# Kernel optimization log

Measured on AMD Instinct MI355X. Metric: run time of the kernel, lower is better.

## Reference

```python
import jax, jax.numpy as jnp
import numpy as np

WS = 5   # window_size
VN = 8   # view_num -> H = W = VN*WS = 40


def _layernorm(x, g, b, eps=1e-5):
    mu = x.mean(-1, keepdims=True)
    var = ((x - mu) ** 2).mean(-1, keepdims=True)
    return (x - mu) * jax.lax.rsqrt(var + eps) * g + b


def _rel_index():
    # standard Swin relative-position index for a WS x WS window
    coords = np.stack(np.meshgrid(np.arange(WS), np.arange(WS), indexing='ij')).reshape(2, -1)
    rel = (coords[:, :, None] - coords[:, None, :]).transpose(1, 2, 0)  # (T,T,2)
    rel = rel + (WS - 1)
    return rel[:, :, 0] * (2 * WS - 1) + rel[:, :, 1]  # (T,T) int


def _attn_mask(H, W):
    # checkerboard mask: outer product of flattened per-window checkerboard,
    # 0 where both positions are 'on', -100 elsewhere (matches masked_fill logic)
    ckbd = np.zeros((H, W), np.float32)
    ckbd[0::2, 1::2] = 1.0
    ckbd[1::2, 0::2] = 1.0
    win = ckbd.reshape(VN, WS, VN, WS).transpose(0, 2, 1, 3).reshape(VN * VN, WS * WS)
    m = win[:, :, None] * win[:, None, :]  # (N,T,T)
    return np.where(m == 0.0, -100.0, 0.0).astype(np.float32)


def setup_inputs() -> dict:
    key = jax.random.key(0)
    ks = jax.random.split(key, 8)
    B, C, H, W = 64, 256, 40, 40
    nh = 8
    dim2 = 2 * C
    hid = int(dim2 * 2.0)

    def n(k, shape, s=0.02):
        return jax.random.normal(k, shape, jnp.float32) * s

    return dict(
        x=jax.random.normal(ks[0], (B, C, H, W), jnp.float32),
        qkv_w=n(ks[1], (C, 3 * C)), qkv_b=jnp.zeros((3 * C,), jnp.float32),
        rel_table=n(ks[2], ((2 * WS - 1) ** 2, nh)),
        proj_w=n(ks[3], (C, dim2)), proj_b=jnp.zeros((dim2,), jnp.float32),
        mlp_w1=n(ks[4], (dim2, hid)), mlp_b1=jnp.zeros((hid,), jnp.float32),
        mlp_w2=n(ks[5], (hid, dim2)), mlp_b2=jnp.zeros((dim2,), jnp.float32),
        norm1_g=jnp.ones((C,), jnp.float32), norm1_b=jnp.zeros((C,), jnp.float32),
        norm2_g=jnp.ones((dim2,), jnp.float32), norm2_b=jnp.zeros((dim2,), jnp.float32),
    )


def reference(x, qkv_w, qkv_b, rel_table, proj_w, proj_b,
              mlp_w1, mlp_b1, mlp_w2, mlp_b2,
              norm1_g, norm1_b, norm2_g, norm2_b):
    B, C, H, W = x.shape
    nh = rel_table.shape[1]
    hd = C // nh
    N = VN * VN           # windows
    T = WS * WS           # tokens per window
    scale = hd ** -0.5

    xs = _layernorm(x.reshape(B, C, H * W).transpose(0, 2, 1), norm1_g, norm1_b)  # (B,L,C)
    qkv = xs @ qkv_w + qkv_b                                   # (B,L,3C)
    qkv = qkv.reshape(B, H, W, 3, C).transpose(3, 0, 4, 1, 2)  # (3,B,C,H,W)
    # windowize: (3,B,C,u,ws,v,ws) -> (3,B,N,C,T)
    qkv = qkv.reshape(3, B, C, VN, WS, VN, WS).transpose(0, 1, 3, 5, 2, 4, 6).reshape(3, B, N, C, T)
    # NOTE: original splits C as (head_dim, num_heads) -- head index is MINOR
    qkv = qkv.reshape(3, B, N, hd, nh, T).transpose(0, 1, 2, 4, 5, 3)  # (3,B,N,nh,T,hd)
    q, k, v = qkv[0] * scale, qkv[1], qkv[2]

    attn = jnp.einsum('bnhtd,bnhsd->bnhts', q, k)              # (B,N,nh,T,T)
    bias = rel_table[jnp.asarray(_rel_index())].transpose(2, 0, 1)  # (nh,T,T)
    mask = jnp.asarray(_attn_mask(H, W))                       # (N,T,T)
    attn = jax.nn.softmax(attn + bias[None, None] + mask[None, :, None], axis=-1)

    out = jnp.einsum('bnhts,bnhsd->bnhtd', attn, v)            # (B,N,nh,T,hd)
    out = out.reshape(B, N, nh, WS, WS, hd).transpose(0, 1, 3, 4, 2, 5)  # (B,N,ws,ws,nh,hd)
    # 'B (u v) h w nh c -> B (u h v w) (nh c)'
    out = out.reshape(B, VN, VN, WS, WS, C).transpose(0, 1, 3, 2, 4, 5).reshape(B, H * W, C)

    y = out @ proj_w + proj_b                                  # (B,L,2C)
    h = _layernorm(y, norm2_g, norm2_b)
    h = jax.nn.gelu(h @ mlp_w1 + mlp_b1, approximate=False) @ mlp_w2 + mlp_b2
    y = y + h
    return y.transpose(0, 2, 1).reshape(B, -1, H, W)           # (B,2C,H,W)
```

## Files before the change

kernel.cpp:

```cpp
#include <hip/hip_runtime.h>
#include <math.h>

#define B_   64
#define C_   256
#define L_   1600
#define T_   25
#define ROWS (B_*L_)
#define QSCALE 0.17677669529663687f

typedef _Float16 f16;
typedef f16 f16x8 __attribute__((ext_vector_type(8)));
typedef f16 f16x4 __attribute__((ext_vector_type(4)));
typedef f16 f16x2 __attribute__((ext_vector_type(2)));
typedef float f32x4 __attribute__((ext_vector_type(4)));

__device__ __forceinline__ void gload_lds16(const void* g, void* l) {
  __builtin_amdgcn_global_load_lds(
      (const __attribute__((address_space(1))) unsigned int*)g,
      (__attribute__((address_space(3))) unsigned int*)l, 16, 0, 0);
}

__device__ __forceinline__ float dot8(f16x8 a, f16x8 b, float acc) {
  union U { f16x8 v; f16x2 p[4]; };
  U ua; ua.v = a;
  U ub; ub.v = b;
#pragma unroll
  for (int i = 0; i < 4; ++i)
    acc = __builtin_amdgcn_fdot2(ua.p[i], ub.p[i], acc, false);
  return acc;
}

__global__ __launch_bounds__(256) void wtrans(const float* __restrict__ w,
                                              f16* __restrict__ o, int K, int N) {
  __shared__ f16 tile[64][72];
  int tid = threadIdx.x;
  int n0 = blockIdx.x * 64, k0 = blockIdx.y * 64;
  int nn = tid & 63, kq = tid >> 6;
#pragma unroll
  for (int i = 0; i < 16; ++i) {
    int k = kq * 16 + i;
    tile[nn][k] = (f16)w[(size_t)(k0 + k) * N + n0 + nn];
  }
  __syncthreads();
#pragma unroll
  for (int jj = 0; jj < 2; ++jj) {
    int e = jj * 256 + tid;
    int nr = e >> 3, kb = e & 7;
    *(f16x8*)&o[(size_t)(n0 + nr) * K + k0 + kb * 8] = *(const f16x8*)&tile[nr][kb * 8];
  }
}

__global__ __launch_bounds__(256) void ln1_fused(const float* __restrict__ x,
    const float* __restrict__ g, const float* __restrict__ be,
    f16* __restrict__ xs) {
  __shared__ float t32[256][65];
  __shared__ float gL[256], beL[256];
  int tid = threadIdx.x;
  gL[tid] = g[tid]; beL[tid] = be[tid];
  int r0 = blockIdx.x * 64;
  int w = tid >> 6, rl = tid & 63;
  int grow = r0 + rl;
  int b = grow / L_, l = grow - b * L_;
  const float* xb = x + (size_t)b * (C_ * L_) + l;
#pragma unroll
  for (int i = 0; i < 64; ++i) {
    int c = w + i * 4;
    t32[c][rl] = xb[(size_t)c * L_];
  }
  __syncthreads();
  int row = tid >> 2, q = tid & 3;
  float s = 0.f, s2 = 0.f;
#pragma unroll
  for (int i = 0; i < 64; ++i) {
    float vv = t32[q * 64 + i][row];
    s += vv; s2 += vv * vv;
  }
  s += __shfl_xor(s, 1); s2 += __shfl_xor(s2, 1);
  s += __shfl_xor(s, 2); s2 += __shfl_xor(s2, 2);
  float m = s * (1.0f / 256.0f);
  float rr = rsqrtf(s2 * (1.0f / 256.0f) - m * m + 1e-5f);
  f16* orow = &xs[(size_t)(r0 + row) * 256 + q * 64];
#pragma unroll
  for (int z8 = 0; z8 < 8; ++z8) {
    f16x8 ov;
#pragma unroll
    for (int z = 0; z < 8; ++z) {
      int c = q * 64 + z8 * 8 + z;
      ov[z] = (f16)((t32[c][row] - m) * rr * gL[c] + beL[c]);
    }
    *(f16x8*)(orow + z8 * 8) = ov;
  }
}

template<int K, int N, int EPI>
__global__ __launch_bounds__(256) void gemm16(
    const f16* __restrict__ A, const f16* __restrict__ BT,
    const float* __restrict__ bias,
    float* __restrict__ outF, f16* __restrict__ outH,
    const f16* __restrict__ resid, int row_off) {
  __shared__ __align__(16) char smem[(EPI == 3) ? 64 * 129 * 4 : 16384];
  f16* As = (f16*)smem;
  f16* Bs = (f16*)(smem + 8192);
  float* tT = (float*)smem;
  int tid = threadIdx.x;
  int w = tid >> 6, lane = tid & 63;
  int wr = w >> 1, wc = w & 1;
  int r0 = blockIdx.y * 128;
  int n0 = blockIdx.x * 128;

  f32x4 acc[4][4] = {};

  for (int k0 = 0; k0 < K; k0 += 32) {
#pragma unroll
    for (int i = 0; i < 2; ++i) {
      int e = i * 256 + tid;
      int row = e >> 2, t = e & 3;
      int cb = t ^ ((row >> 1) & 3);
      gload_lds16(A + (size_t)(r0 + row) * K + k0 + cb * 8,
                  &As[(i * 4 + w) * 512]);
    }
#pragma unroll
    for (int i = 0; i < 2; ++i) {
      int e = i * 256 + tid;
      int row = e >> 2, t = e & 3;
      int cb = t ^ ((row >> 1) & 3);
      gload_lds16(BT + (size_t)(n0 + row) * K + k0 + cb * 8,
                  &Bs[(i * 4 + w) * 512]);
    }
    __syncthreads();

    f16x8 af[4], bf[4];
#pragma unroll
    for (int m = 0; m < 4; ++m) {
      int ar = wr * 64 + m * 16 + (lane & 15);
      int sl = (lane >> 4) ^ ((ar >> 1) & 3);
      af[m] = *(const f16x8*)&As[ar * 32 + sl * 8];
    }
#pragma unroll
    for (int n = 0; n < 4; ++n) {
      int br = wc * 64 + n * 16 + (lane & 15);
      int sl = (lane >> 4) ^ ((br >> 1) & 3);
      bf[n] = *(const f16x8*)&Bs[br * 32 + sl * 8];
    }
#pragma unroll
    for (int m = 0; m < 4; ++m)
#pragma unroll
      for (int n = 0; n < 4; ++n)
        acc[m][n] = __builtin_amdgcn_mfma_f32_16x16x32_f16(af[m], bf[n], acc[m][n], 0, 0, 0);
    __syncthreads();
  }

  if constexpr (EPI != 3) {
#pragma unroll
    for (int m = 0; m < 4; ++m) {
#pragma unroll
      for (int n = 0; n < 4; ++n) {
        int gcol = n0 + wc * 64 + n * 16 + (lane & 15);
        float bb = bias[gcol];
#pragma unroll
        for (int j = 0; j < 4; ++j) {
          int grow = r0 + wr * 64 + m * 16 + ((lane >> 4) << 2) + j;
          float v = acc[m][n][j] + bb;
          if constexpr (EPI == 0) {
            outH[(size_t)grow * N + gcol] = (f16)v;
          } else {
            float gl = 0.5f * v * (1.0f + erff(v * 0.70710678118654752f));
            outH[(size_t)grow * N + gcol] = (f16)gl;
          }
        }
      }
    }
  } else {
    for (int p = 0; p < 2; ++p) {
      if (wr == p) {
#pragma unroll
        for (int m = 0; m < 4; ++m) {
          int lr = m * 16 + ((lane >> 4) << 2);
#pragma unroll
          for (int n = 0; n < 4; ++n) {
            int lc = wc * 64 + n * 16 + (lane & 15);
            int gcol = n0 + lc;
            float bb = bias[gcol];
#pragma unroll
            for (int j = 0; j < 4; ++j) {
              int grow = row_off + r0 + p * 64 + lr + j;
              tT[(lr + j) * 129 + lc] =
                  acc[m][n][j] + bb + (float)resid[(size_t)grow * 512 + gcol];
            }
          }
        }
      }
      __syncthreads();
#pragma unroll
      for (int it = 0; it < 8; ++it) {
        int idx = it * 256 + tid;
        int col = idx >> 4;
        int r4 = idx & 15;
        int grow0 = row_off + r0 + p * 64 + r4 * 4;
        int b = grow0 / L_;
        int l = grow0 - b * L_;
        float4 o = make_float4(tT[(r4 * 4 + 0) * 129 + col],
                               tT[(r4 * 4 + 1) * 129 + col],
                               tT[(r4 * 4 + 2) * 129 + col],
                               tT[(r4 * 4 + 3) * 129 + col]);
        *(float4*)&outF[((size_t)b * 512 + n0 + col) * L_ + l] = o;
      }
      __syncthreads();
    }
  }
}

#define PST 776
__global__ __launch_bounds__(256) void attn_kernel(const f16* __restrict__ qkv,
                                                   const float* __restrict__ rel,
                                                   f16* __restrict__ outp) {
  __shared__ f16 qc[T_][PST];
  __shared__ f16 relL[81 * 8];
  int tid = threadIdx.x;
  int bn = blockIdx.x;
  int b = bn >> 6, n = bn & 63;
  int u = n >> 3, v = n & 7;

  for (int e = tid; e < 648; e += 256) relL[e] = (f16)rel[e];

  for (int e = tid; e < T_ * 96; e += 256) {
    int t = e / 96;
    int g = e - t * 96;
    int i = t / 5, j = t - i * 5;
    int l = (u * 5 + i) * 40 + v * 5 + j;
    f16x8 val = *(const f16x8*)&qkv[(size_t)(b * L_ + l) * 768 + g * 8];
    int which = g >> 5;
    int d = g & 31;
    int base = which * 256 + d;
#pragma unroll
    for (int h = 0; h < 8; ++h)
      qc[t][base + h * 32] = val[h];
  }
  __syncthreads();

  int h = tid >> 5, t = tid & 31;
  if (t < T_) {
    int i1 = t / 5, j1 = t - i1 * 5;
    int par1 = (u + v + i1 + j1) & 1;
    const f16* qp = &qc[t][h * 32];
    f16x8 q0 = *(const f16x8*)(qp + 0);
    f16x8 q1 = *(const f16x8*)(qp + 8);
    f16x8 q2 = *(const f16x8*)(qp + 16);
    f16x8 q3 = *(const f16x8*)(qp + 24);

    float p[T_];
    float mx = -1e30f;
#pragma unroll
    for (int s = 0; s < T_; ++s) {
      int i2 = s / 5, j2 = s - i2 * 5;
      const f16* kp = &qc[s][256 + h * 32];
      f16x8 k0 = *(const f16x8*)(kp + 0);
      f16x8 k1 = *(const f16x8*)(kp + 8);
      f16x8 k2 = *(const f16x8*)(kp + 16);
      f16x8 k3 = *(const f16x8*)(kp + 24);
      float d0 = 0.f, d1 = 0.f;
      d0 = dot8(q0, k0, d0);
      d1 = dot8(q1, k1, d1);
      d0 = dot8(q2, k2, d0);
      d1 = dot8(q3, k3, d1);
      float bias = (float)relL[((i1 - i2 + 4) * 9 + (j1 - j2 + 4)) * 8 + h];
      int par2 = (u + v + i2 + j2) & 1;
      float sc = (d0 + d1) * QSCALE + bias + ((par1 & par2) ? 0.0f : -100.0f);
      p[s] = sc;
      mx = fmaxf(mx, sc);
    }
    float sum = 0.f;
#pragma unroll
    for (int s = 0; s < T_; ++s) {
      float e = __expf(p[s] - mx);
      p[s] = e;
      sum += e;
    }
    float inv = 1.0f / sum;
#pragma unroll
    for (int s = 0; s < T_; ++s) p[s] *= inv;

    int l = (u * 5 + i1) * 40 + v * 5 + j1;
    f16* op = &outp[(size_t)(b * L_ + l) * 256 + h * 32];

#pragma unroll
    for (int half = 0; half < 2; ++half) {
      float acc[16] = {};
#pragma unroll
      for (int s = 0; s < T_; ++s) {
        const f16* vp = &qc[s][512 + h * 32 + half * 16];
        f16x8 v0 = *(const f16x8*)(vp + 0);
        f16x8 v1 = *(const f16x8*)(vp + 8);
        float ps = p[s];
#pragma unroll
        for (int z = 0; z < 8; ++z) {
          acc[z]     += ps * (float)v0[z];
          acc[8 + z] += ps * (float)v1[z];
        }
      }
#pragma unroll
      for (int z8 = 0; z8 < 2; ++z8) {
        f16x8 ov;
#pragma unroll
        for (int z = 0; z < 8; ++z) ov[z] = (f16)acc[z8 * 8 + z];
        *(f16x8*)(op + half * 16 + z8 * 8) = ov;
      }
    }
  }
}

__global__ __launch_bounds__(256) void ln2_fused(const f16* __restrict__ y,
    const float* __restrict__ g, const float* __restrict__ be,
    f16* __restrict__ yln) {
  int wv = threadIdx.x >> 6, lane = threadIdx.x & 63;
  int row = blockIdx.x * 4 + wv;
  const f16x8* yp = (const f16x8*)(y + (size_t)row * 512);
  f16x8 h0 = yp[lane];
  float v[8];
  float s = 0.f, s2 = 0.f;
#pragma unroll
  for (int z = 0; z < 8; ++z) {
    v[z] = (float)h0[z];
    s += v[z]; s2 += v[z] * v[z];
  }
#pragma unroll
  for (int o = 32; o; o >>= 1) { s += __shfl_xor(s, o); s2 += __shfl_xor(s2, o); }
  float m = s * (1.0f / 512.0f);
  float rr = rsqrtf(s2 * (1.0f / 512.0f) - m * m + 1e-5f);
  float4 g0 = ((const float4*)g)[lane * 2], g1 = ((const float4*)g)[lane * 2 + 1];
  float4 b0 = ((const float4*)be)[lane * 2], b1 = ((const float4*)be)[lane * 2 + 1];
  float gg[8] = {g0.x, g0.y, g0.z, g0.w, g1.x, g1.y, g1.z, g1.w};
  float bb[8] = {b0.x, b0.y, b0.z, b0.w, b1.x, b1.y, b1.z, b1.w};
  f16x8 o8;
#pragma unroll
  for (int z = 0; z < 8; ++z)
    o8[z] = (f16)((v[z] - m) * rr * gg[z] + bb[z]);
  *(f16x8*)&yln[(size_t)row * 512 + lane * 8] = o8;
}

extern "C" void kernel_launch(void* const* d_in, const int* in_sizes, int n_in,
                              void* d_out, int out_size, void* d_ws, size_t ws_size,
                              hipStream_t stream) {
  const float* x      = (const float*)d_in[0];
  const float* qkv_w  = (const float*)d_in[1];
  const float* qkv_b  = (const float*)d_in[2];
  const float* rel    = (const float*)d_in[3];
  const float* proj_w = (const float*)d_in[4];
  const float* proj_b = (const float*)d_in[5];
  const float* w1     = (const float*)d_in[6];
  const float* b1     = (const float*)d_in[7];
  const float* w2     = (const float*)d_in[8];
  const float* b2     = (const float*)d_in[9];
  const float* g1     = (const float*)d_in[10];
  const float* be1    = (const float*)d_in[11];
  const float* g2     = (const float*)d_in[12];
  const float* be2    = (const float*)d_in[13];
  float* out = (float*)d_out;

  char* w8 = (char*)d_ws;
  f16* qkv_wT  = (f16*)(w8 + 1638400);
  f16* proj_wT = qkv_wT + 768 * 256;
  f16* w1T     = proj_wT + 512 * 256;
  f16* w2T     = w1T + 1024 * 512;
  char* P0 = w8 + 4390912;
  f16* qkv_h = (f16*)P0;
  f16* y_h   = (f16*)P0;
  char* P1 = P0 + (size_t)ROWS * 768 * 2;
  f16* xs_h  = (f16*)P1;
  f16* att_h = (f16*)(P1 + (size_t)ROWS * 256 * 2);
  f16* yln   = (f16*)P1;
  char* P2 = P1 + (size_t)ROWS * 512 * 2;
  f16* hid = (f16*)P2;

  size_t need_full = 4390912 + (size_t)ROWS * 768 * 2 + (size_t)ROWS * 512 * 2
                   + (size_t)ROWS * 1024 * 2;
  bool full = ws_size >= need_full;

  wtrans<<<dim3(768 / 64, 256 / 64), 256, 0, stream>>>(qkv_w, qkv_wT, 256, 768);
  wtrans<<<dim3(512 / 64, 256 / 64), 256, 0, stream>>>(proj_w, proj_wT, 256, 512);
  wtrans<<<dim3(1024 / 64, 512 / 64), 256, 0, stream>>>(w1, w1T, 512, 1024);
  wtrans<<<dim3(512 / 64, 1024 / 64), 256, 0, stream>>>(w2, w2T, 1024, 512);

  ln1_fused<<<ROWS / 64, 256, 0, stream>>>(x, g1, be1, xs_h);

  gemm16<256, 768, 0><<<dim3(6, ROWS / 128), 256, 0, stream>>>(
      xs_h, qkv_wT, qkv_b, nullptr, qkv_h, nullptr, 0);

  attn_kernel<<<B_ * 64, 256, 0, stream>>>(qkv_h, rel, att_h);

  gemm16<256, 512, 0><<<dim3(4, ROWS / 128), 256, 0, stream>>>(
      att_h, proj_wT, proj_b, nullptr, y_h, nullptr, 0);

  ln2_fused<<<ROWS / 4, 256, 0, stream>>>(y_h, g2, be2, yln);

  if (full) {
    gemm16<512, 1024, 2><<<dim3(8, ROWS / 128), 256, 0, stream>>>(
        yln, w1T, b1, nullptr, hid, nullptr, 0);
    gemm16<1024, 512, 3><<<dim3(4, ROWS / 128), 256, 0, stream>>>(
        hid, w2T, b2, out, nullptr, y_h, 0);
  } else {
    const int CHUNK = ROWS / 4;
    for (int c = 0; c < 4; ++c) {
      int off = c * CHUNK;
      gemm16<512, 1024, 2><<<dim3(8, CHUNK / 128), 256, 0, stream>>>(
          yln + (size_t)off * 512, w1T, b1, nullptr, hid, nullptr, 0);
      gemm16<1024, 512, 3><<<dim3(4, CHUNK / 128), 256, 0, stream>>>(
          hid, w2T, b2, out, nullptr, y_h, off);
    }
  }
  (void)in_sizes; (void)n_in; (void)out_size;
}
```

Measured before the change: 783.1 us.

## Use 8-wave GEMM blocks with XCD-aware tile swizzle for L2 reuse

The fp16 MFMA GEMM now runs 512 threads per block. Each of the 8 waves computes a 64x32 sub-tile instead of 4 waves computing 64x64, so each thread issues a single LDS-direct load per operand per k-step. The 2D grid becomes a 1D grid that is remapped so consecutive blocks on the same XCD share a row tile. The goal is better reuse of the A operand in each XCD's L2 and more waves to hide latency. The trade-off is fewer MFMAs per fragment load per wave, which lowers register-level reuse.

```diff
diff --git a/kernel.cpp b/kernel.cpp
--- a/kernel.cpp
+++ b/kernel.cpp
@@ -92,44 +92,35 @@
   }
 }
 
-template<int K, int N, int EPI>
-__global__ __launch_bounds__(256) void gemm16(
+template<int K, int N, int EPI, int NCB>
+__global__ __launch_bounds__(512) void gemm16(
     const f16* __restrict__ A, const f16* __restrict__ BT,
     const float* __restrict__ bias,
     float* __restrict__ outF, f16* __restrict__ outH,
-    const f16* __restrict__ resid, int row_off) {
+    const f16* __restrict__ resid, int row_off, int nrp8) {
   __shared__ __align__(16) char smem[(EPI == 3) ? 64 * 129 * 4 : 16384];
   f16* As = (f16*)smem;
   f16* Bs = (f16*)(smem + 8192);
   float* tT = (float*)smem;
   int tid = threadIdx.x;
   int w = tid >> 6, lane = tid & 63;
-  int wr = w >> 1, wc = w & 1;
-  int r0 = blockIdx.y * 128;
-  int n0 = blockIdx.x * 128;
-
-  f32x4 acc[4][4] = {};
+  int wr = w >> 2, wc = w & 3;
+  int bid = blockIdx.x;
+  int xcd = bid & 7, j1d = bid >> 3;
+  int member = j1d % NCB, grp = j1d / NCB;
+  int r0 = (xcd * nrp8 + grp) * 128;
+  int n0 = member * 128;
+
+  f32x4 acc[4][2] = {};
+  int srow = tid >> 2, st = tid & 3;
+  int scb = st ^ ((srow >> 1) & 3);
 
   for (int k0 = 0; k0 < K; k0 += 32) {
-#pragma unroll
-    for (int i = 0; i < 2; ++i) {
-      int e = i * 256 + tid;
-      int row = e >> 2, t = e & 3;
-      int cb = t ^ ((row >> 1) & 3);
-      gload_lds16(A + (size_t)(r0 + row) * K + k0 + cb * 8,
-                  &As[(i * 4 + w) * 512]);
-    }
-#pragma unroll
-    for (int i = 0; i < 2; ++i) {
-      int e = i * 256 + tid;
-      int row = e >> 2, t = e & 3;
-      int cb = t ^ ((row >> 1) & 3);
-      gload_lds16(BT + (size_t)(n0 + row) * K + k0 + cb * 8,
-                  &Bs[(i * 4 + w) * 512]);
-    }
+    gload_lds16(A + (size_t)(r0 + srow) * K + k0 + scb * 8, &As[w * 512]);
+    gload_lds16(BT + (size_t)(n0 + srow) * K + k0 + scb * 8, &Bs[w * 512]);
     __syncthreads();
 
-    f16x8 af[4], bf[4];
+    f16x8 af[4], bf[2];
 #pragma unroll
     for (int m = 0; m < 4; ++m) {
       int ar = wr * 64 + m * 16 + (lane & 15);
@@ -137,15 +128,15 @@
       af[m] = *(const f16x8*)&As[ar * 32 + sl * 8];
     }
 #pragma unroll
-    for (int n = 0; n < 4; ++n) {
-      int br = wc * 64 + n * 16 + (lane & 15);
+    for (int n = 0; n < 2; ++n) {
+      int br = wc * 32 + n * 16 + (lane & 15);
       int sl = (lane >> 4) ^ ((br >> 1) & 3);
       bf[n] = *(const f16x8*)&Bs[br * 32 + sl * 8];
     }
 #pragma unroll
     for (int m = 0; m < 4; ++m)
 #pragma unroll
-      for (int n = 0; n < 4; ++n)
+      for (int n = 0; n < 2; ++n)
         acc[m][n] = __builtin_amdgcn_mfma_f32_16x16x32_f16(af[m], bf[n], acc[m][n], 0, 0, 0);
     __syncthreads();
   }
@@ -154,17 +145,17 @@
 #pragma unroll
     for (int m = 0; m < 4; ++m) {
 #pragma unroll
-      for (int n = 0; n < 4; ++n) {
-        int gcol = n0 + wc * 64 + n * 16 + (lane & 15);
+      for (int n = 0; n < 2; ++n) {
+        int gcol = n0 + wc * 32 + n * 16 + (lane & 15);
         float bb = bias[gcol];
 #pragma unroll
-        for (int j = 0; j < 4; ++j) {
-          int grow = r0 + wr * 64 + m * 16 + ((lane >> 4) << 2) + j;
-          float v = acc[m][n][j] + bb;
+        for (int j2 = 0; j2 < 4; ++j2) {
+          int grow = r0 + wr * 64 + m * 16 + ((lane >> 4) << 2) + j2;
+          float vv = acc[m][n][j2] + bb;
           if constexpr (EPI == 0) {
-            outH[(size_t)grow * N + gcol] = (f16)v;
+            outH[(size_t)grow * N + gcol] = (f16)vv;
           } else {
-            float gl = 0.5f * v * (1.0f + erff(v * 0.70710678118654752f));
+            float gl = 0.5f * vv * (1.0f + erff(vv * 0.70710678118654752f));
             outH[(size_t)grow * N + gcol] = (f16)gl;
           }
         }
@@ -177,23 +168,23 @@
         for (int m = 0; m < 4; ++m) {
           int lr = m * 16 + ((lane >> 4) << 2);
 #pragma unroll
-          for (int n = 0; n < 4; ++n) {
-            int lc = wc * 64 + n * 16 + (lane & 15);
+          for (int n = 0; n < 2; ++n) {
+            int lc = wc * 32 + n * 16 + (lane & 15);
             int gcol = n0 + lc;
             float bb = bias[gcol];
 #pragma unroll
-            for (int j = 0; j < 4; ++j) {
-              int grow = row_off + r0 + p * 64 + lr + j;
-              tT[(lr + j) * 129 + lc] =
-                  acc[m][n][j] + bb + (float)resid[(size_t)grow * 512 + gcol];
+            for (int j2 = 0; j2 < 4; ++j2) {
+              int grow = row_off + r0 + p * 64 + lr + j2;
+              tT[(lr + j2) * 129 + lc] =
+                  acc[m][n][j2] + bb + (float)resid[(size_t)grow * 512 + gcol];
             }
           }
         }
       }
       __syncthreads();
 #pragma unroll
-      for (int it = 0; it < 8; ++it) {
-        int idx = it * 256 + tid;
+      for (int it = 0; it < 4; ++it) {
+        int idx = it * 512 + tid;
         int col = idx >> 4;
         int r4 = idx & 15;
         int grow0 = row_off + r0 + p * 64 + r4 * 4;
@@ -383,29 +374,29 @@
 
   ln1_fused<<<ROWS / 64, 256, 0, stream>>>(x, g1, be1, xs_h);
 
-  gemm16<256, 768, 0><<<dim3(6, ROWS / 128), 256, 0, stream>>>(
-      xs_h, qkv_wT, qkv_b, nullptr, qkv_h, nullptr, 0);
+  gemm16<256, 768, 0, 6><<<6 * (ROWS / 128), 512, 0, stream>>>(
+      xs_h, qkv_wT, qkv_b, nullptr, qkv_h, nullptr, 0, (ROWS / 128) / 8);
 
   attn_kernel<<<B_ * 64, 256, 0, stream>>>(qkv_h, rel, att_h);
 
-  gemm16<256, 512, 0><<<dim3(4, ROWS / 128), 256, 0, stream>>>(
-      att_h, proj_wT, proj_b, nullptr, y_h, nullptr, 0);
+  gemm16<256, 512, 0, 4><<<4 * (ROWS / 128), 512, 0, stream>>>(
+      att_h, proj_wT, proj_b, nullptr, y_h, nullptr, 0, (ROWS / 128) / 8);
 
   ln2_fused<<<ROWS / 4, 256, 0, stream>>>(y_h, g2, be2, yln);
 
   if (full) {
-    gemm16<512, 1024, 2><<<dim3(8, ROWS / 128), 256, 0, stream>>>(
-        yln, w1T, b1, nullptr, hid, nullptr, 0);
-    gemm16<1024, 512, 3><<<dim3(4, ROWS / 128), 256, 0, stream>>>(
-        hid, w2T, b2, out, nullptr, y_h, 0);
+    gemm16<512, 1024, 2, 8><<<8 * (ROWS / 128), 512, 0, stream>>>(
+        yln, w1T, b1, nullptr, hid, nullptr, 0, (ROWS / 128) / 8);
+    gemm16<1024, 512, 3, 4><<<4 * (ROWS / 128), 512, 0, stream>>>(
+        hid, w2T, b2, out, nullptr, y_h, 0, (ROWS / 128) / 8);
   } else {
     const int CHUNK = ROWS / 4;
     for (int c = 0; c < 4; ++c) {
       int off = c * CHUNK;
-      gemm16<512, 1024, 2><<<dim3(8, CHUNK / 128), 256, 0, stream>>>(
-          yln + (size_t)off * 512, w1T, b1, nullptr, hid, nullptr, 0);
-      gemm16<1024, 512, 3><<<dim3(4, CHUNK / 128), 256, 0, stream>>>(
-          hid, w2T, b2, out, nullptr, y_h, off);
+      gemm16<512, 1024, 2, 8><<<8 * (CHUNK / 128), 512, 0, stream>>>(
+          yln + (size_t)off * 512, w1T, b1, nullptr, hid, nullptr, off, (CHUNK / 128) / 8);
+      gemm16<1024, 512, 3, 4><<<4 * (CHUNK / 128), 512, 0, stream>>>(
+          hid, w2T, b2, out, nullptr, y_h, off, (CHUNK / 128) / 8);
     }
   }
   (void)in_sizes; (void)n_in; (void)out_size;
```

Result: faster. 745.2 us (-4.8%).
